# Optimization experiments

Measured on AMD Instinct MI355X. Metric: run time of the kernel, lower is better.

## Reference

```python
import jax, jax.numpy as jnp
import numpy as np

NUM_EDGE_TYPES = 38
NUM_NODE_TYPES = 4
HIDDEN = 64
HOPS = 4
N_NODES = 100_000
N_EDGES = 1_600_000


def setup_inputs() -> dict:
    key = jax.random.key(0)
    ks = jax.random.split(key, 7)
    in_dim = NUM_EDGE_TYPES + 2 * NUM_NODE_TYPES  # 46
    return {
        "edge_index": jax.random.randint(ks[0], (2, N_EDGES), 0, N_NODES),
        "edge_type": jax.random.randint(ks[1], (N_EDGES,), 0, NUM_EDGE_TYPES),
        "node_type": jax.random.randint(ks[2], (N_NODES,), 0, NUM_NODE_TYPES),
        "W1": jax.random.normal(ks[3], (in_dim, HIDDEN), dtype=jnp.float32) * 0.1,
        "b1": jax.random.normal(ks[4], (HIDDEN,), dtype=jnp.float32) * 0.1,
        "W2": jax.random.normal(ks[5], (HIDDEN, 1), dtype=jnp.float32) * 0.1,
        "b2": jax.random.normal(ks[6], (1,), dtype=jnp.float32) * 0.1,
    }


def reference(edge_index, edge_type, node_type, W1, b1, W2, b2):
    src, dst = edge_index[0], edge_index[1]  # PyG: x_j = x[edge_index[0]], aggregate at edge_index[1]
    head_type = node_type[src]
    tail_type = node_type[dst]
    # Linear over concat of three one-hots == sum of three gathered weight rows + bias.
    h = (W1[edge_type]
         + W1[NUM_EDGE_TYPES + head_type]
         + W1[NUM_EDGE_TYPES + NUM_NODE_TYPES + tail_type]
         + b1)                                   # [E, HIDDEN]
    h = jax.nn.gelu(h)
    edge_emb = jax.nn.sigmoid(h @ W2 + b2)       # [E, 1]

    num_nodes = node_type.shape[0]
    aggr = jnp.zeros((num_nodes, 1), dtype=edge_emb.dtype)
    for _ in range(HOPS):
        msg = aggr[src] + edge_emb               # gather + add, [E, 1]
        aggr = jax.ops.segment_sum(msg, dst, num_segments=num_nodes)  # scatter-add
    return aggr
```

## Files before the change

### kernel.cpp

```cpp
#include <hip/hip_runtime.h>

#define NUM_EDGE_TYPES 38
#define NUM_NODE_TYPES 4
#define HIDDEN 64
#define TABLE_SIZE (NUM_EDGE_TYPES * NUM_NODE_TYPES * NUM_NODE_TYPES)
#define SRC_BITS 17
#define SRC_MASK ((1 << SRC_BITS) - 1)
#define BSHIFT 8
#define BNODES 256
#define MAXB 512
#define PB 512
#define CHUNK (PB * 8)
#define CAPC 6144

__device__ __forceinline__ float table_entry(int i, const float* __restrict__ W1,
                                             const float* __restrict__ b1,
                                             const float* __restrict__ W2,
                                             const float* __restrict__ b2) {
    int et = i >> 4, ht = (i >> 2) & 3, tt = i & 3;
    const float* r0 = W1 + et * HIDDEN;
    const float* r1 = W1 + (NUM_EDGE_TYPES + ht) * HIDDEN;
    const float* r2 = W1 + (NUM_EDGE_TYPES + NUM_NODE_TYPES + tt) * HIDDEN;
    float acc = b2[0];
#pragma unroll 8
    for (int k = 0; k < HIDDEN; ++k) {
        float h = r0[k] + r1[k] + r2[k] + b1[k];
        float u = 0.7978845608028654f * (h + 0.044715f * h * h * h);
        float g = 0.5f * h * (1.0f + tanhf(u));
        acc += g * W2[k];
    }
    return 1.0f / (1.0f + expf(-acc));
}

__global__ void init_kernel(const float* __restrict__ W1, const float* __restrict__ b1,
                            const float* __restrict__ W2, const float* __restrict__ b2,
                            float* __restrict__ table, int* __restrict__ cursor) {
    int t = threadIdx.x;
    if (t < MAXB) cursor[t] = 0;
    if (t < TABLE_SIZE) table[t] = table_entry(t, W1, b1, W2, b2);
}

__global__ void table_kernel(const float* __restrict__ W1, const float* __restrict__ b1,
                             const float* __restrict__ W2, const float* __restrict__ b2,
                             float* __restrict__ table) {
    int i = blockIdx.x * blockDim.x + threadIdx.x;
    if (i < TABLE_SIZE) table[i] = table_entry(i, W1, b1, W2, b2);
}

__global__ void partition_kernel(const int* __restrict__ src, const int* __restrict__ dst,
                                 const int* __restrict__ etype, int* __restrict__ cursor,
                                 int* __restrict__ pack, int E, int nbk, int cap) {
    __shared__ int hist[MAXB];
    __shared__ int locCur[MAXB];
    for (int i = threadIdx.x; i < nbk; i += PB) hist[i] = 0;
    __syncthreads();
    int start = blockIdx.x * CHUNK;
    int end = min(start + CHUNK, E);
    if (end - start == CHUNK) {
        int j0 = start + threadIdx.x * 4;
        int j1 = start + PB * 4 + threadIdx.x * 4;
        int4 da = *(const int4*)(dst + j0);
        int4 db = *(const int4*)(dst + j1);
        atomicAdd(&hist[da.x >> BSHIFT], 1);
        atomicAdd(&hist[da.y >> BSHIFT], 1);
        atomicAdd(&hist[da.z >> BSHIFT], 1);
        atomicAdd(&hist[da.w >> BSHIFT], 1);
        atomicAdd(&hist[db.x >> BSHIFT], 1);
        atomicAdd(&hist[db.y >> BSHIFT], 1);
        atomicAdd(&hist[db.z >> BSHIFT], 1);
        atomicAdd(&hist[db.w >> BSHIFT], 1);
        int4 sa = *(const int4*)(src + j0);
        int4 sb = *(const int4*)(src + j1);
        int4 ea = *(const int4*)(etype + j0);
        int4 eb = *(const int4*)(etype + j1);
        __syncthreads();
        for (int i = threadIdx.x; i < nbk; i += PB) {
            int h = hist[i];
            locCur[i] = h ? i * cap + atomicAdd(&cursor[i], h) : 0;
        }
        __syncthreads();
        int t0 = atomicAdd(&locCur[da.x >> BSHIFT], 1);
        int t1 = atomicAdd(&locCur[da.y >> BSHIFT], 1);
        int t2 = atomicAdd(&locCur[da.z >> BSHIFT], 1);
        int t3 = atomicAdd(&locCur[da.w >> BSHIFT], 1);
        int t4 = atomicAdd(&locCur[db.x >> BSHIFT], 1);
        int t5 = atomicAdd(&locCur[db.y >> BSHIFT], 1);
        int t6 = atomicAdd(&locCur[db.z >> BSHIFT], 1);
        int t7 = atomicAdd(&locCur[db.w >> BSHIFT], 1);
        pack[t0] = (ea.x << (SRC_BITS + 8)) | ((da.x & (BNODES - 1)) << SRC_BITS) | sa.x;
        pack[t1] = (ea.y << (SRC_BITS + 8)) | ((da.y & (BNODES - 1)) << SRC_BITS) | sa.y;
        pack[t2] = (ea.z << (SRC_BITS + 8)) | ((da.z & (BNODES - 1)) << SRC_BITS) | sa.z;
        pack[t3] = (ea.w << (SRC_BITS + 8)) | ((da.w & (BNODES - 1)) << SRC_BITS) | sa.w;
        pack[t4] = (eb.x << (SRC_BITS + 8)) | ((db.x & (BNODES - 1)) << SRC_BITS) | sb.x;
        pack[t5] = (eb.y << (SRC_BITS + 8)) | ((db.y & (BNODES - 1)) << SRC_BITS) | sb.y;
        pack[t6] = (eb.z << (SRC_BITS + 8)) | ((db.z & (BNODES - 1)) << SRC_BITS) | sb.z;
        pack[t7] = (eb.w << (SRC_BITS + 8)) | ((db.w & (BNODES - 1)) << SRC_BITS) | sb.w;
    } else {
        for (int j = start + threadIdx.x; j < end; j += PB)
            atomicAdd(&hist[dst[j] >> BSHIFT], 1);
        __syncthreads();
        for (int i = threadIdx.x; i < nbk; i += PB) {
            int h = hist[i];
            locCur[i] = h ? i * cap + atomicAdd(&cursor[i], h) : 0;
        }
        __syncthreads();
        for (int j = start + threadIdx.x; j < end; j += PB) {
            int d = dst[j];
            int slot = atomicAdd(&locCur[d >> BSHIFT], 1);
            pack[slot] = (etype[j] << (SRC_BITS + 8)) | ((d & (BNODES - 1)) << SRC_BITS) | src[j];
        }
    }
}

__global__ __launch_bounds__(512)
void base_lds_kernel(const int* __restrict__ pack, const int* __restrict__ cursor,
                     const int* __restrict__ ntype, const float* __restrict__ table,
                     float* __restrict__ base, int N, int cap) {
    __shared__ float tbl[TABLE_SIZE];
    __shared__ float accL[BNODES];
    __shared__ unsigned char ntLoc[BNODES];
    int b = blockIdx.x;
    int tid = threadIdx.x;
    int node0 = b << BSHIFT;
    int st = b * cap;
    int c = min(cursor[b], cap);

    for (int i = tid; i < TABLE_SIZE; i += 512) tbl[i] = table[i];
    if (tid < BNODES) {
        accL[tid] = 0.0f;
        int n = node0 + tid;
        ntLoc[tid] = (n < N) ? (unsigned char)ntype[n] : (unsigned char)0;
    }
    __syncthreads();

    int c4 = c & ~3;
    for (int j = tid * 4; j < c4; j += 512 * 4) {
        int4 v = *(const int4*)(pack + st + j);
        int s0 = v.x & SRC_MASK, s1 = v.y & SRC_MASK;
        int s2 = v.z & SRC_MASK, s3 = v.w & SRC_MASK;
        int h0 = ntype[s0], h1 = ntype[s1], h2 = ntype[s2], h3 = ntype[s3];
        int d0 = (v.x >> SRC_BITS) & (BNODES - 1);
        int d1 = (v.y >> SRC_BITS) & (BNODES - 1);
        int d2 = (v.z >> SRC_BITS) & (BNODES - 1);
        int d3 = (v.w >> SRC_BITS) & (BNODES - 1);
        atomicAdd(&accL[d0], tbl[(int)((((unsigned)v.x) >> (SRC_BITS + 8)) << 4) | (h0 << 2) | (int)ntLoc[d0]]);
        atomicAdd(&accL[d1], tbl[(int)((((unsigned)v.y) >> (SRC_BITS + 8)) << 4) | (h1 << 2) | (int)ntLoc[d1]]);
        atomicAdd(&accL[d2], tbl[(int)((((unsigned)v.z) >> (SRC_BITS + 8)) << 4) | (h2 << 2) | (int)ntLoc[d2]]);
        atomicAdd(&accL[d3], tbl[(int)((((unsigned)v.w) >> (SRC_BITS + 8)) << 4) | (h3 << 2) | (int)ntLoc[d3]]);
    }
    for (int j = c4 + tid; j < c; j += 512) {
        int p = pack[st + j];
        int dl = (p >> SRC_BITS) & (BNODES - 1);
        int h = ntype[p & SRC_MASK];
        atomicAdd(&accL[dl], tbl[(int)((((unsigned)p) >> (SRC_BITS + 8)) << 4) | (h << 2) | (int)ntLoc[dl]]);
    }
    __syncthreads();
    if (tid < BNODES) {
        int n = node0 + tid;
        if (n < N) base[n] = accL[tid];
    }
}

__global__ __launch_bounds__(512)
void hop_lds_kernel(const int* __restrict__ pack, const int* __restrict__ cursor,
                    const float* __restrict__ base, const float* __restrict__ prev,
                    float* __restrict__ out, int N, int cap) {
    __shared__ float accL[BNODES];
    int b = blockIdx.x;
    int tid = threadIdx.x;
    int node0 = b << BSHIFT;
    int st = b * cap;
    int c = min(cursor[b], cap);
    if (tid < BNODES) accL[tid] = 0.0f;
    __syncthreads();

    int c4 = c & ~3;
    for (int j = tid * 4; j < c4; j += 512 * 4) {
        int4 v = *(const int4*)(pack + st + j);
        float g0 = prev[v.x & SRC_MASK];
        float g1 = prev[v.y & SRC_MASK];
        float g2 = prev[v.z & SRC_MASK];
        float g3 = prev[v.w & SRC_MASK];
        atomicAdd(&accL[(v.x >> SRC_BITS) & (BNODES - 1)], g0);
        atomicAdd(&accL[(v.y >> SRC_BITS) & (BNODES - 1)], g1);
        atomicAdd(&accL[(v.z >> SRC_BITS) & (BNODES - 1)], g2);
        atomicAdd(&accL[(v.w >> SRC_BITS) & (BNODES - 1)], g3);
    }
    for (int j = c4 + tid; j < c; j += 512) {
        int p = pack[st + j];
        atomicAdd(&accL[(p >> SRC_BITS) & (BNODES - 1)], prev[p & SRC_MASK]);
    }
    __syncthreads();
    if (tid < BNODES) {
        int n = node0 + tid;
        if (n < N) out[n] = base[n] + accL[tid];
    }
}

__global__ void edge_base_kernel(const int* __restrict__ src, const int* __restrict__ dst,
                                 const int* __restrict__ etype, const int* __restrict__ ntype,
                                 const float* __restrict__ table, float* __restrict__ base, int E) {
    __shared__ float tbl[TABLE_SIZE];
    for (int i = threadIdx.x; i < TABLE_SIZE; i += blockDim.x) tbl[i] = table[i];
    __syncthreads();
    int e = blockIdx.x * blockDim.x + threadIdx.x;
    if (e >= E) return;
    int s = src[e];
    int d = dst[e];
    int idx = (etype[e] << 4) | (ntype[s] << 2) | ntype[d];
    atomicAdd(base + d, tbl[idx]);
}

__global__ void copy_kernel(const float* __restrict__ in, float* __restrict__ out, int N) {
    int i = blockIdx.x * blockDim.x + threadIdx.x;
    if (i < N) out[i] = in[i];
}

__global__ void edge_hop_kernel(const int* __restrict__ src, const int* __restrict__ dst,
                                const float* __restrict__ prev, float* __restrict__ next, int E) {
    int e = blockIdx.x * blockDim.x + threadIdx.x;
    if (e >= E) return;
    atomicAdd(next + dst[e], prev[src[e]]);
}

extern "C" void kernel_launch(void* const* d_in, const int* in_sizes, int n_in,
                              void* d_out, int out_size, void* d_ws, size_t ws_size,
                              hipStream_t stream) {
    const int* edge_index = (const int*)d_in[0];
    const int* etype      = (const int*)d_in[1];
    const int* ntype      = (const int*)d_in[2];
    const float* W1       = (const float*)d_in[3];
    const float* b1       = (const float*)d_in[4];
    const float* W2       = (const float*)d_in[5];
    const float* b2       = (const float*)d_in[6];

    const int E = in_sizes[1];
    const int N = in_sizes[2];
    const int* src = edge_index;
    const int* dst = edge_index + E;
    float* out = (float*)d_out;

    const int nbk = (N + BNODES - 1) >> BSHIFT;
    const int nChunks = (E + CHUNK - 1) / CHUNK;

    int cap = ((E / (nbk > 0 ? nbk : 1)) * 3 / 2 + 255) & ~255;
    if (cap < 512) cap = 512;
    size_t packElems = (size_t)nbk * cap;

    size_t need = (packElems + MAXB + 1024 + (size_t)3 * N) * 4 + 256;

    if (ws_size >= need && nbk <= MAXB && cap <= CAPC) {
        int* pack     = (int*)d_ws;
        int* cursor   = pack + packElems;
        float* table  = (float*)(cursor + MAXB);
        float* base   = table + 1024;
        float* bufA   = base + N;
        float* bufB   = bufA + N;

        init_kernel<<<1, 1024, 0, stream>>>(W1, b1, W2, b2, table, cursor);
        partition_kernel<<<nChunks, PB, 0, stream>>>(src, dst, etype, cursor, pack, E, nbk, cap);
        base_lds_kernel<<<nbk, 512, 0, stream>>>(pack, cursor, ntype, table, base, N, cap);
        hop_lds_kernel<<<nbk, 512, 0, stream>>>(pack, cursor, base, base, bufA, N, cap);
        hop_lds_kernel<<<nbk, 512, 0, stream>>>(pack, cursor, base, bufA, bufB, N, cap);
        hop_lds_kernel<<<nbk, 512, 0, stream>>>(pack, cursor, base, bufB, out, N, cap);
    } else {
        float* table = (float*)d_ws;
        float* base  = table + 1024;
        float* bufA  = base + N;
        float* bufB  = bufA + N;
        const int eb = (E + 255) / 256;
        const int nb = (N + 255) / 256;

        hipMemsetAsync(base, 0, (size_t)N * sizeof(float), stream);
        table_kernel<<<(TABLE_SIZE + 255) / 256, 256, 0, stream>>>(W1, b1, W2, b2, table);

        edge_base_kernel<<<eb, 256, 0, stream>>>(src, dst, etype, ntype, table, base, E);
        copy_kernel<<<nb, 256, 0, stream>>>(base, bufA, N);
        edge_hop_kernel<<<eb, 256, 0, stream>>>(src, dst, base, bufA, E);
        copy_kernel<<<nb, 256, 0, stream>>>(base, bufB, N);
        edge_hop_kernel<<<eb, 256, 0, stream>>>(src, dst, bufA, bufB, E);
        copy_kernel<<<nb, 256, 0, stream>>>(base, out, N);
        edge_hop_kernel<<<eb, 256, 0, stream>>>(src, dst, bufB, out, E);
    }
}
```

Baseline: 157.3 us.

## Halve destination bucket size and fold table build into partition kernel

```diff
diff --git a/kernel.cpp b/kernel.cpp
--- a/kernel.cpp
+++ b/kernel.cpp
@@ -6,9 +6,10 @@
 #define TABLE_SIZE (NUM_EDGE_TYPES * NUM_NODE_TYPES * NUM_NODE_TYPES)
 #define SRC_BITS 17
 #define SRC_MASK ((1 << SRC_BITS) - 1)
-#define BSHIFT 8
-#define BNODES 256
-#define MAXB 512
+#define BSHIFT 7
+#define BNODES 128
+#define ETSHIFT (SRC_BITS + BSHIFT)
+#define MAXB 1024
 #define PB 512
 #define CHUNK (PB * 8)
 #define CAPC 6144
@@ -32,14 +33,6 @@
     return 1.0f / (1.0f + expf(-acc));
 }
 
-__global__ void init_kernel(const float* __restrict__ W1, const float* __restrict__ b1,
-                            const float* __restrict__ W2, const float* __restrict__ b2,
-                            float* __restrict__ table, int* __restrict__ cursor) {
-    int t = threadIdx.x;
-    if (t < MAXB) cursor[t] = 0;
-    if (t < TABLE_SIZE) table[t] = table_entry(t, W1, b1, W2, b2);
-}
-
 __global__ void table_kernel(const float* __restrict__ W1, const float* __restrict__ b1,
                              const float* __restrict__ W2, const float* __restrict__ b2,
                              float* __restrict__ table) {
@@ -49,7 +42,10 @@
 
 __global__ void partition_kernel(const int* __restrict__ src, const int* __restrict__ dst,
                                  const int* __restrict__ etype, int* __restrict__ cursor,
-                                 int* __restrict__ pack, int E, int nbk, int cap) {
+                                 int* __restrict__ pack, int E, int nbk, int cap,
+                                 const float* __restrict__ W1, const float* __restrict__ b1,
+                                 const float* __restrict__ W2, const float* __restrict__ b2,
+                                 float* __restrict__ table) {
     __shared__ int hist[MAXB];
     __shared__ int locCur[MAXB];
     for (int i = threadIdx.x; i < nbk; i += PB) hist[i] = 0;
@@ -87,14 +83,14 @@
         int t5 = atomicAdd(&locCur[db.y >> BSHIFT], 1);
         int t6 = atomicAdd(&locCur[db.z >> BSHIFT], 1);
         int t7 = atomicAdd(&locCur[db.w >> BSHIFT], 1);
-        pack[t0] = (ea.x << (SRC_BITS + 8)) | ((da.x & (BNODES - 1)) << SRC_BITS) | sa.x;
-        pack[t1] = (ea.y << (SRC_BITS + 8)) | ((da.y & (BNODES - 1)) << SRC_BITS) | sa.y;
-        pack[t2] = (ea.z << (SRC_BITS + 8)) | ((da.z & (BNODES - 1)) << SRC_BITS) | sa.z;
-        pack[t3] = (ea.w << (SRC_BITS + 8)) | ((da.w & (BNODES - 1)) << SRC_BITS) | sa.w;
-        pack[t4] = (eb.x << (SRC_BITS + 8)) | ((db.x & (BNODES - 1)) << SRC_BITS) | sb.x;
-        pack[t5] = (eb.y << (SRC_BITS + 8)) | ((db.y & (BNODES - 1)) << SRC_BITS) | sb.y;
-        pack[t6] = (eb.z << (SRC_BITS + 8)) | ((db.z & (BNODES - 1)) << SRC_BITS) | sb.z;
-        pack[t7] = (eb.w << (SRC_BITS + 8)) | ((db.w & (BNODES - 1)) << SRC_BITS) | sb.w;
+        pack[t0] = (ea.x << ETSHIFT) | ((da.x & (BNODES - 1)) << SRC_BITS) | sa.x;
+        pack[t1] = (ea.y << ETSHIFT) | ((da.y & (BNODES - 1)) << SRC_BITS) | sa.y;
+        pack[t2] = (ea.z << ETSHIFT) | ((da.z & (BNODES - 1)) << SRC_BITS) | sa.z;
+        pack[t3] = (ea.w << ETSHIFT) | ((da.w & (BNODES - 1)) << SRC_BITS) | sa.w;
+        pack[t4] = (eb.x << ETSHIFT) | ((db.x & (BNODES - 1)) << SRC_BITS) | sb.x;
+        pack[t5] = (eb.y << ETSHIFT) | ((db.y & (BNODES - 1)) << SRC_BITS) | sb.y;
+        pack[t6] = (eb.z << ETSHIFT) | ((db.z & (BNODES - 1)) << SRC_BITS) | sb.z;
+        pack[t7] = (eb.w << ETSHIFT) | ((db.w & (BNODES - 1)) << SRC_BITS) | sb.w;
     } else {
         for (int j = start + threadIdx.x; j < end; j += PB)
             atomicAdd(&hist[dst[j] >> BSHIFT], 1);
@@ -107,7 +103,28 @@
         for (int j = start + threadIdx.x; j < end; j += PB) {
             int d = dst[j];
             int slot = atomicAdd(&locCur[d >> BSHIFT], 1);
-            pack[slot] = (etype[j] << (SRC_BITS + 8)) | ((d & (BNODES - 1)) << SRC_BITS) | src[j];
+            pack[slot] = (etype[j] << ETSHIFT) | ((d & (BNODES - 1)) << SRC_BITS) | src[j];
+        }
+    }
+
+    if (blockIdx.x == 0) {
+        int wid = threadIdx.x >> 6, lane = threadIdx.x & 63;
+        for (int e = wid; e < TABLE_SIZE; e += PB / 64) {
+            int et = e >> 4, ht = (e >> 2) & 3, tt = e & 3;
+            float h = W1[et * HIDDEN + lane]
+                    + W1[(NUM_EDGE_TYPES + ht) * HIDDEN + lane]
+                    + W1[(NUM_EDGE_TYPES + NUM_NODE_TYPES + tt) * HIDDEN + lane]
+                    + b1[lane];
+            float u = 0.7978845608028654f * (h + 0.044715f * h * h * h);
+            float g = 0.5f * h * (1.0f + tanhf(u));
+            float v = g * W2[lane];
+            v += __shfl_xor(v, 32, 64);
+            v += __shfl_xor(v, 16, 64);
+            v += __shfl_xor(v, 8, 64);
+            v += __shfl_xor(v, 4, 64);
+            v += __shfl_xor(v, 2, 64);
+            v += __shfl_xor(v, 1, 64);
+            if (lane == 0) table[e] = 1.0f / (1.0f + expf(-(v + b2[0])));
         }
     }
 }
@@ -136,23 +153,22 @@
     int c4 = c & ~3;
     for (int j = tid * 4; j < c4; j += 512 * 4) {
         int4 v = *(const int4*)(pack + st + j);
-        int s0 = v.x & SRC_MASK, s1 = v.y & SRC_MASK;
-        int s2 = v.z & SRC_MASK, s3 = v.w & SRC_MASK;
-        int h0 = ntype[s0], h1 = ntype[s1], h2 = ntype[s2], h3 = ntype[s3];
+        int h0 = ntype[v.x & SRC_MASK], h1 = ntype[v.y & SRC_MASK];
+        int h2 = ntype[v.z & SRC_MASK], h3 = ntype[v.w & SRC_MASK];
         int d0 = (v.x >> SRC_BITS) & (BNODES - 1);
         int d1 = (v.y >> SRC_BITS) & (BNODES - 1);
         int d2 = (v.z >> SRC_BITS) & (BNODES - 1);
         int d3 = (v.w >> SRC_BITS) & (BNODES - 1);
-        atomicAdd(&accL[d0], tbl[(int)((((unsigned)v.x) >> (SRC_BITS + 8)) << 4) | (h0 << 2) | (int)ntLoc[d0]]);
-        atomicAdd(&accL[d1], tbl[(int)((((unsigned)v.y) >> (SRC_BITS + 8)) << 4) | (h1 << 2) | (int)ntLoc[d1]]);
-        atomicAdd(&accL[d2], tbl[(int)((((unsigned)v.z) >> (SRC_BITS + 8)) << 4) | (h2 << 2) | (int)ntLoc[d2]]);
-        atomicAdd(&accL[d3], tbl[(int)((((unsigned)v.w) >> (SRC_BITS + 8)) << 4) | (h3 << 2) | (int)ntLoc[d3]]);
+        atomicAdd(&accL[d0], tbl[(int)(((unsigned)v.x) >> ETSHIFT << 4) | (h0 << 2) | (int)ntLoc[d0]]);
+        atomicAdd(&accL[d1], tbl[(int)(((unsigned)v.y) >> ETSHIFT << 4) | (h1 << 2) | (int)ntLoc[d1]]);
+        atomicAdd(&accL[d2], tbl[(int)(((unsigned)v.z) >> ETSHIFT << 4) | (h2 << 2) | (int)ntLoc[d2]]);
+        atomicAdd(&accL[d3], tbl[(int)(((unsigned)v.w) >> ETSHIFT << 4) | (h3 << 2) | (int)ntLoc[d3]]);
     }
     for (int j = c4 + tid; j < c; j += 512) {
         int p = pack[st + j];
         int dl = (p >> SRC_BITS) & (BNODES - 1);
         int h = ntype[p & SRC_MASK];
-        atomicAdd(&accL[dl], tbl[(int)((((unsigned)p) >> (SRC_BITS + 8)) << 4) | (h << 2) | (int)ntLoc[dl]]);
+        atomicAdd(&accL[dl], tbl[(int)(((unsigned)p) >> ETSHIFT << 4) | (h << 2) | (int)ntLoc[dl]]);
     }
     __syncthreads();
     if (tid < BNODES) {
@@ -257,8 +273,9 @@
         float* bufA   = base + N;
         float* bufB   = bufA + N;
 
-        init_kernel<<<1, 1024, 0, stream>>>(W1, b1, W2, b2, table, cursor);
-        partition_kernel<<<nChunks, PB, 0, stream>>>(src, dst, etype, cursor, pack, E, nbk, cap);
+        hipMemsetAsync(cursor, 0, MAXB * sizeof(int), stream);
+        partition_kernel<<<nChunks, PB, 0, stream>>>(src, dst, etype, cursor, pack, E, nbk, cap,
+                                                     W1, b1, W2, b2, table);
         base_lds_kernel<<<nbk, 512, 0, stream>>>(pack, cursor, ntype, table, base, N, cap);
         hop_lds_kernel<<<nbk, 512, 0, stream>>>(pack, cursor, base, base, bufA, N, cap);
         hop_lds_kernel<<<nbk, 512, 0, stream>>>(pack, cursor, base, bufA, bufB, N, cap);
```

After: 189.4 us. +20.3%, slower.
